# Optimization experiments

Hardware: AMD Instinct MI355X
Metric: run time of the kernel (lower is better)

The kernel has to match this reference:

```python
import jax, jax.numpy as jnp
import numpy as np

N_NODES = 100000
N_EDGES = 1000000
N_GRAPHS = 512
IN_N, IN_E, HID, OUT = 32, 16, 64, 64
EPS = 0.1  # GINEConv eps buffer (not trainable)


def _mlp2(x, w0, b0, w1, b1):
    # 2-layer MLP: Linear -> ReLU -> Linear
    return jax.nn.relu(x @ w0 + b0) @ w1 + b1


def setup_inputs() -> dict:
    key = jax.random.key(0)
    ks = jax.random.split(key, 24)
    s = 0.05
    inp = {
        "x": jax.random.normal(ks[0], (N_NODES, IN_N), jnp.float32),
        "edge_index": jax.random.randint(ks[1], (2, N_EDGES), 0, N_NODES, jnp.int32),
        "edge_attr": jax.random.normal(ks[2], (N_EDGES, IN_E), jnp.float32),
        "batch": jnp.sort(jax.random.randint(ks[3], (N_NODES,), 0, N_GRAPHS, jnp.int32)),
        # node init MLP
        "wn0": jax.random.normal(ks[4], (IN_N, HID)) * s, "bn0": jnp.zeros((HID,)),
        "wn1": jax.random.normal(ks[5], (HID, HID)) * s, "bn1": jnp.zeros((HID,)),
        # edge init MLP
        "we0": jax.random.normal(ks[6], (IN_E, HID)) * s, "be0": jnp.zeros((HID,)),
        "we1": jax.random.normal(ks[7], (HID, HID)) * s, "be1": jnp.zeros((HID,)),
        # 3 residual GINE convs, MLP weights stacked on leading layer axis
        "cw0": jax.random.normal(ks[8], (3, HID, HID)) * s, "cb0": jnp.zeros((3, HID)),
        "cw1": jax.random.normal(ks[9], (3, HID, HID)) * s, "cb1": jnp.zeros((3, HID)),
        # final GINE conv MLP (hidden -> out)
        "lw0": jax.random.normal(ks[10], (HID, HID)) * s, "lb0": jnp.zeros((HID,)),
        "lw1": jax.random.normal(ks[11], (HID, OUT)) * s, "lb1": jnp.zeros((OUT,)),
    }
    return inp


def _gine_conv(x, src, dst, e, w0, b0, w1, b1):
    # message = relu(x_j + edge_attr); aggregate = scatter-add at target i
    msg = jax.nn.relu(x[src] + e)                       # [E, H]
    agg = jax.ops.segment_sum(msg, dst, num_segments=x.shape[0])  # [N, H]
    out = agg + (1.0 + EPS) * x
    return _mlp2(out, w0, b0, w1, b1)


def reference(x, edge_index, edge_attr, batch,
              wn0, bn0, wn1, bn1, we0, be0, we1, be1,
              cw0, cb0, cw1, cb1, lw0, lb0, lw1, lb1):
    src, dst = edge_index[0], edge_index[1]
    h = _mlp2(x, wn0, bn0, wn1, bn1)          # [N, HID]
    e = _mlp2(edge_attr, we0, be0, we1, be1)  # [E, HID]
    for l in range(3):  # residual GINE layers (BatchNorm never applied in source forward)
        h = jax.nn.relu(h + _gine_conv(h, src, dst, e, cw0[l], cb0[l], cw1[l], cb1[l]))
    h = _gine_conv(h, src, dst, e, lw0, lb0, lw1, lb1)  # [N, OUT]
    return jax.ops.segment_sum(h, batch, num_segments=N_GRAPHS)  # global_add_pool -> [G, OUT]
```

## Files before the change

### kernel.cpp

```cpp
#include <hip/hip_runtime.h>
#include <hip/hip_bf16.h>
#include <stdint.h>

#define N_NODES 100000
#define N_EDGES 1000000
#define N_GRAPHS 512
#define HID 64
#define INN 32
#define INE 16
#define CPAD 32

#define NPB 256
#define NBKT ((N_NODES + NPB - 1) / NPB)
#define BCAP 4096

typedef unsigned int uint32;
typedef unsigned short ushort16;
typedef __attribute__((ext_vector_type(8))) short bf8;
typedef __attribute__((ext_vector_type(4))) float f32x4;

__device__ __forceinline__ ushort16 f2bf(float f) {
    uint32 u = __float_as_uint(f);
    uint32 r = (u + 0x7fffu + ((u >> 16) & 1u)) >> 16;
    return (ushort16)r;
}
__device__ __forceinline__ uint32 pack_bf2(float lo, float hi) {
    return (uint32)f2bf(lo) | ((uint32)f2bf(hi) << 16);
}
__device__ __forceinline__ float bf_lo(uint32 v) { return __uint_as_float(v << 16); }
__device__ __forceinline__ float bf_hi(uint32 v) { return __uint_as_float(v & 0xffff0000u); }


__global__ void k_diag(float* out, float val) { out[threadIdx.x] = val; }


__global__ __launch_bounds__(256) void k_binA(const int* __restrict__ src,
                                              const int* __restrict__ dst,
                                              int* __restrict__ bcursor,
                                              uint2* __restrict__ binned) {
    __shared__ int cnt[NBKT];
    __shared__ int cur[NBKT];
    const int t = threadIdx.x;
    for (int b = t; b < NBKT; b += 256) cnt[b] = 0;
    __syncthreads();
    const int base = blockIdx.x * 4096;
    #pragma unroll
    for (int j = 0; j < 16; j++) {
        int e = base + j * 256 + t;
        if (e < N_EDGES) atomicAdd(&cnt[dst[e] >> 8], 1);
    }
    __syncthreads();
    for (int b = t; b < NBKT; b += 256) {
        int c = cnt[b];
        cur[b] = (c > 0) ? atomicAdd(&bcursor[(size_t)b * CPAD], c) : 0;
    }
    __syncthreads();
    #pragma unroll
    for (int j = 0; j < 16; j++) {
        int e = base + j * 256 + t;
        if (e < N_EDGES) {
            int d = dst[e];
            int bkt = d >> 8;
            int r = atomicAdd(&cur[bkt], 1);
            if (r < BCAP)
                binned[(size_t)bkt * BCAP + r] =
                    make_uint2((uint32)src[e] | ((uint32)(d & (NPB - 1)) << 17), (uint32)e);
        }
    }
}

__global__ __launch_bounds__(512) void k_scanB(const int* __restrict__ bcursor,
                                               int* __restrict__ bbase) {
    __shared__ int sh[512];
    const int t = threadIdx.x;
    int v = (t < NBKT) ? min(bcursor[(size_t)t * CPAD], BCAP) : 0;
    sh[t] = v; __syncthreads();
    for (int off = 1; off < 512; off <<= 1) {
        int u = (t >= off) ? sh[t - off] : 0;
        __syncthreads();
        sh[t] += u;
        __syncthreads();
    }
    if (t < NBKT) bbase[t] = sh[t] - v;
}

__global__ __launch_bounds__(256) void k_bucketB(const int* __restrict__ bcursor,
                                                 const int* __restrict__ bbase,
                                                 const uint2* __restrict__ binned,
                                                 int* __restrict__ rowptr,
                                                 int* __restrict__ perm_src,
                                                 int* __restrict__ eperm) {
    __shared__ int cnt[NPB];
    __shared__ int sh[NPB];
    const int b = blockIdx.x, t = threadIdx.x;
    const int n = min(bcursor[(size_t)b * CPAD], BCAP);
    const int base = bbase[b];
    const uint2* brec = binned + (size_t)b * BCAP;
    cnt[t] = 0;
    __syncthreads();
    for (int i = t; i < n; i += 256)
        atomicAdd(&cnt[brec[i].x >> 17], 1);
    __syncthreads();
    int c = cnt[t];
    sh[t] = c; __syncthreads();
    for (int off = 1; off < NPB; off <<= 1) {
        int u = (t >= off) ? sh[t - off] : 0;
        __syncthreads();
        sh[t] += u;
        __syncthreads();
    }
    int excl = sh[t] - c;
    int g = b * NPB + t;
    if (g < N_NODES) rowptr[g] = base + excl;
    if (b == 0 && t == 0) rowptr[N_NODES] = N_EDGES;
    cnt[t] = excl;
    __syncthreads();
    for (int i = t; i < n; i += 256) {
        uint2 r = brec[i];
        int dl = (int)(r.x >> 17);
        int p = base + atomicAdd(&cnt[dl], 1);
        perm_src[p] = (int)(r.x & 0x1FFFFu);
        eperm[p] = (int)r.y;
    }
}


template<int K0, bool RELU_RES, bool BF_IN>
__global__ __launch_bounds__(256, 3) void k_mlp_mfma(
    const void* __restrict__ in, const float* __restrict__ hprev, float* __restrict__ out,
    const float* __restrict__ w0, const float* __restrict__ b0,
    const float* __restrict__ w1, const float* __restrict__ b1,
    uint32* __restrict__ out_bf, int nrows)
{
    constexpr int NF = K0 / 32;
    __shared__ ushort tile[4][16 * 72];
    const int wave = threadIdx.x >> 6, lane = threadIdx.x & 63;
    const int quad = lane >> 4, mn = lane & 15;
    ushort* T = &tile[wave][0];

    bf8 w0f[4][NF];
    #pragma unroll
    for (int t = 0; t < 4; t++)
        #pragma unroll
        for (int f = 0; f < NF; f++)
            #pragma unroll
            for (int j = 0; j < 8; j++) {
                int k = f * 32 + quad * 8 + j;
                w0f[t][f][j] = (short)f2bf(w0[k * HID + t * 16 + mn]);
            }
    bf8 w1f[4][2];
    #pragma unroll
    for (int t = 0; t < 4; t++)
        #pragma unroll
        for (int f = 0; f < 2; f++)
            #pragma unroll
            for (int j = 0; j < 8; j++) {
                int k = f * 32 + quad * 8 + j;
                w1f[t][f][j] = (short)f2bf(w1[k * HID + t * 16 + mn]);
            }
    float b0v[4], b1v[4];
    #pragma unroll
    for (int t = 0; t < 4; t++) { b0v[t] = b0[t*16+mn]; b1v[t] = b1[t*16+mn]; }

    const int ebase = blockIdx.x * 64 + wave * 16;
    int rowA = ebase + mn; if (rowA > nrows - 1) rowA = nrows - 1;
    bf8 a1[NF];
    if (BF_IN) {
        const ushort* row = (const ushort*)in + (size_t)rowA * HID;
        #pragma unroll
        for (int f = 0; f < NF; f++)
            a1[f] = *(const bf8*)(row + f * 32 + quad * 8);
    } else {
        const float* inf = (const float*)in;
        #pragma unroll
        for (int f = 0; f < NF; f++) {
            const float4* pr = (const float4*)(inf + (size_t)rowA * K0 + f * 32 + quad * 8);
            float4 v0 = pr[0], v1 = pr[1];
            a1[f][0]=(short)f2bf(v0.x); a1[f][1]=(short)f2bf(v0.y);
            a1[f][2]=(short)f2bf(v0.z); a1[f][3]=(short)f2bf(v0.w);
            a1[f][4]=(short)f2bf(v1.x); a1[f][5]=(short)f2bf(v1.y);
            a1[f][6]=(short)f2bf(v1.z); a1[f][7]=(short)f2bf(v1.w);
        }
    }
    #pragma unroll
    for (int t = 0; t < 4; t++) {
        f32x4 c = {0.f, 0.f, 0.f, 0.f};
        #pragma unroll
        for (int f = 0; f < NF; f++)
            c = __builtin_amdgcn_mfma_f32_16x16x32_bf16(a1[f], w0f[t][f], c, 0, 0, 0);
        #pragma unroll
        for (int rg = 0; rg < 4; rg++) {
            int row = quad * 4 + rg;
            T[row * 72 + t * 16 + mn] = f2bf(fmaxf(c[rg] + b0v[t], 0.f));
        }
    }
    __syncthreads();
    bf8 a2[2];
    #pragma unroll
    for (int f = 0; f < 2; f++)
        a2[f] = *(const bf8*)&T[mn * 72 + f * 32 + quad * 8];
    #pragma unroll
    for (int t = 0; t < 4; t++) {
        f32x4 c = {0.f, 0.f, 0.f, 0.f};
        c = __builtin_amdgcn_mfma_f32_16x16x32_bf16(a2[0], w1f[t][0], c, 0, 0, 0);
        c = __builtin_amdgcn_mfma_f32_16x16x32_bf16(a2[1], w1f[t][1], c, 0, 0, 0);
        #pragma unroll
        for (int rg = 0; rg < 4; rg++) {
            int row = quad * 4 + rg;
            int rowg = ebase + row;
            int rowc = (rowg < nrows) ? rowg : (nrows - 1);
            float v = c[rg] + b1v[t];
            if (RELU_RES) {
                float hv = hprev[(size_t)rowc * HID + t * 16 + mn];
                v = fmaxf(v + hv, 0.f);
            }
            if (rowg < nrows) out[(size_t)rowg * HID + t * 16 + mn] = v;
            T[row * 72 + t * 16 + mn] = f2bf(v);
        }
    }
    if (out_bf) {
        __syncthreads();
        int half = lane >> 5, c32 = lane & 31;
        #pragma unroll
        for (int rr = 0; rr < 8; rr++) {
            int row = rr * 2 + half;
            int pos = ebase + row;
            if (pos < nrows) {
                uint32 lo = T[row * 72 + c32 * 2];
                uint32 hi = T[row * 72 + c32 * 2 + 1];
                out_bf[(size_t)pos * 32 + c32] = lo | (hi << 16);
            }
        }
    }
}


__global__ __launch_bounds__(256, 4) void k_edge_mlp_mfma(
    const float* __restrict__ eattr, const int* __restrict__ eperm,
    uint32* __restrict__ e_sorted,
    const float* __restrict__ w0, const float* __restrict__ b0,
    const float* __restrict__ w1, const float* __restrict__ b1)
{
    __shared__ ushort tile[4][16 * 72];
    const int wave = threadIdx.x >> 6, lane = threadIdx.x & 63;
    const int quad = lane >> 4, mn = lane & 15;
    ushort* T = &tile[wave][0];

    bf8 w0f[4];
    #pragma unroll
    for (int t = 0; t < 4; t++) {
        #pragma unroll
        for (int j = 0; j < 8; j++) {
            int k = quad * 8 + j;
            float v = (k < INE) ? w0[k * HID + t * 16 + mn] : 0.f;
            w0f[t][j] = (short)f2bf(v);
        }
    }
    bf8 w1f[4][2];
    #pragma unroll
    for (int t = 0; t < 4; t++)
        #pragma unroll
        for (int f = 0; f < 2; f++)
            #pragma unroll
            for (int j = 0; j < 8; j++) {
                int k = f * 32 + quad * 8 + j;
                w1f[t][f][j] = (short)f2bf(w1[k * HID + t * 16 + mn]);
            }
    float b0v[4], b1v[4];
    #pragma unroll
    for (int t = 0; t < 4; t++) { b0v[t] = b0[t*16+mn]; b1v[t] = b1[t*16+mn]; }

    const int nChunks = N_EDGES / 64;
    for (int chunk = blockIdx.x; chunk < nChunks; chunk += gridDim.x) {
        const int ebase = chunk * 64 + wave * 16;
        const int erow = eperm[ebase + mn];
        bf8 a1 = {};
        if (quad < 2) {
            const float4* pr = (const float4*)(eattr + (size_t)erow * INE + quad * 8);
            float4 v0 = pr[0], v1 = pr[1];
            a1[0]=(short)f2bf(v0.x); a1[1]=(short)f2bf(v0.y);
            a1[2]=(short)f2bf(v0.z); a1[3]=(short)f2bf(v0.w);
            a1[4]=(short)f2bf(v1.x); a1[5]=(short)f2bf(v1.y);
            a1[6]=(short)f2bf(v1.z); a1[7]=(short)f2bf(v1.w);
        }
        #pragma unroll
        for (int t = 0; t < 4; t++) {
            f32x4 c = {0.f, 0.f, 0.f, 0.f};
            c = __builtin_amdgcn_mfma_f32_16x16x32_bf16(a1, w0f[t], c, 0, 0, 0);
            #pragma unroll
            for (int rg = 0; rg < 4; rg++) {
                int row = quad * 4 + rg;
                T[row * 72 + t * 16 + mn] = f2bf(fmaxf(c[rg] + b0v[t], 0.f));
            }
        }
        __syncthreads();
        bf8 a2[2];
        #pragma unroll
        for (int f = 0; f < 2; f++)
            a2[f] = *(const bf8*)&T[mn * 72 + f * 32 + quad * 8];
        #pragma unroll
        for (int t = 0; t < 4; t++) {
            f32x4 c = {0.f, 0.f, 0.f, 0.f};
            c = __builtin_amdgcn_mfma_f32_16x16x32_bf16(a2[0], w1f[t][0], c, 0, 0, 0);
            c = __builtin_amdgcn_mfma_f32_16x16x32_bf16(a2[1], w1f[t][1], c, 0, 0, 0);
            #pragma unroll
            for (int rg = 0; rg < 4; rg++) {
                int row = quad * 4 + rg;
                T[row * 72 + t * 16 + mn] = f2bf(c[rg] + b1v[t]);
            }
        }
        __syncthreads();
        int half = lane >> 5, c32 = lane & 31;
        #pragma unroll
        for (int rr = 0; rr < 8; rr++) {
            int row = rr * 2 + half;
            int drow = ebase + row;
            uint32 lo = T[row * 72 + c32 * 2];
            uint32 hi = T[row * 72 + c32 * 2 + 1];
            e_sorted[(size_t)drow * 32 + c32] = lo | (hi << 16);
        }
        __syncthreads();
    }
}


__global__ __launch_bounds__(256, 4) void k_agg(
    const float* __restrict__ h, const uint32* __restrict__ h_bf,
    const uint32* __restrict__ e_sorted,
    const int* __restrict__ rowptr, const int* __restrict__ perm_src,
    uint32* __restrict__ z_bf)
{
    int node = blockIdx.x * 4 + (threadIdx.x >> 6);
    if (node >= N_NODES) return;
    int lane = threadIdx.x & 63;
    int half = lane >> 5, c = lane & 31;
    int r0 = rowptr[node], r1 = rowptr[node + 1];
    const float2 hn = *(const float2*)&h[(size_t)node * HID + 2*c];
    float accx = 0.f, accy = 0.f;
    #pragma unroll 1
    for (int base = r0; base < r1; base += 16) {
        int idxs[8]; int sidx[8];
        #pragma unroll
        for (int j = 0; j < 8; j++) {
            int idx = base + 2*j + half;
            idxs[j] = idx;
            int idxc = (idx < r1) ? idx : (r1 - 1);
            sidx[j] = perm_src[idxc];
        }
        uint32 hv[8], ev[8];
        #pragma unroll
        for (int j = 0; j < 8; j++) {
            int idxc = (idxs[j] < r1) ? idxs[j] : (r1 - 1);
            hv[j] = h_bf[(size_t)sidx[j] * 32 + c];
            ev[j] = e_sorted[(size_t)idxc * 32 + c];
        }
        #pragma unroll
        for (int j = 0; j < 8; j++) {
            float mx = fmaxf(bf_lo(hv[j]) + bf_lo(ev[j]), 0.f);
            float my = fmaxf(bf_hi(hv[j]) + bf_hi(ev[j]), 0.f);
            if (idxs[j] < r1) { accx += mx; accy += my; }
        }
    }
    accx += __shfl_xor(accx, 32);
    accy += __shfl_xor(accy, 32);
    if (half == 0) {
        float rx = fmaf(1.1f, hn.x, accx);
        float ry = fmaf(1.1f, hn.y, accy);
        z_bf[(size_t)node * 32 + c] = pack_bf2(rx, ry);
    }
}


__global__ __launch_bounds__(256) void k_pool(
    const float* __restrict__ h, const int* __restrict__ batch, float* __restrict__ out)
{
    int g = blockIdx.x;
    int lane = threadIdx.x & 63, wave = threadIdx.x >> 6;
    int lo = 0, hi = N_NODES;
    while (lo < hi) { int mid = (lo + hi) >> 1; if (batch[mid] < g) lo = mid + 1; else hi = mid; }
    int start = lo;
    hi = N_NODES;
    while (lo < hi) { int mid = (lo + hi) >> 1; if (batch[mid] < g + 1) lo = mid + 1; else hi = mid; }
    int end = lo;
    float acc = 0.f;
    for (int n = start + wave; n < end; n += 4)
        acc += h[(size_t)n*HID + lane];
    __shared__ float sh[4][64];
    sh[wave][lane] = acc;
    __syncthreads();
    if (wave == 0)
        out[(size_t)g*HID + lane] = sh[0][lane] + sh[1][lane] + sh[2][lane] + sh[3][lane];
}


extern "C" void kernel_launch(void* const* d_in, const int* in_sizes, int n_in,
                              void* d_out, int out_size, void* d_ws, size_t ws_size,
                              hipStream_t stream) {
    const float* x     = (const float*)d_in[0];
    const int*   eidx  = (const int*)  d_in[1];
    const float* eattr = (const float*)d_in[2];
    const int*   batch = (const int*)  d_in[3];
    const float* wn0 = (const float*)d_in[4];  const float* bn0 = (const float*)d_in[5];
    const float* wn1 = (const float*)d_in[6];  const float* bn1 = (const float*)d_in[7];
    const float* we0 = (const float*)d_in[8];  const float* be0 = (const float*)d_in[9];
    const float* we1 = (const float*)d_in[10]; const float* be1 = (const float*)d_in[11];
    const float* cw0 = (const float*)d_in[12]; const float* cb0 = (const float*)d_in[13];
    const float* cw1 = (const float*)d_in[14]; const float* cb1 = (const float*)d_in[15];
    const float* lw0 = (const float*)d_in[16]; const float* lb0 = (const float*)d_in[17];
    const float* lw1 = (const float*)d_in[18]; const float* lb1 = (const float*)d_in[19];
    const int* src = eidx;
    const int* dst = eidx + N_EDGES;

    char* ws = (char*)d_ws;
    size_t off = 0;
    auto alloc = [&](size_t bytes) -> void* {
        void* p = ws + off;
        off = (off + bytes + 255) & ~(size_t)255;
        return p;
    };
    int*    bcursor  = (int*)  alloc((size_t)NBKT * CPAD * 4);
    int*    bbase    = (int*)  alloc((size_t)NBKT * 4);
    uint2*  binned   = (uint2*)alloc((size_t)NBKT * BCAP * 8);
    int*    rowptr   = (int*)  alloc((size_t)(N_NODES + 1) * 4);
    int*    perm_src = (int*)  alloc((size_t)N_EDGES * 4);
    int*    eperm    = (int*)  alloc((size_t)N_EDGES * 4);
    float*  h        = (float*)alloc((size_t)N_NODES * HID * 4);
    uint32* z_bf     = (uint32*)alloc((size_t)N_NODES * 32 * 4);
    uint32* h_bf     = (uint32*)alloc((size_t)N_NODES * 32 * 4);
    uint32* e_sorted = (uint32*)alloc((size_t)N_EDGES * HID * 2);
    if (off > ws_size) {
        k_diag<<<1, 64, 0, stream>>>((float*)d_out, 1.0e9f);
        return;
    }

    hipMemsetAsync(bcursor, 0, (size_t)NBKT * CPAD * 4, stream);
    k_binA<<<(N_EDGES + 4095) / 4096, 256, 0, stream>>>(src, dst, bcursor, binned);
    k_scanB<<<1, 512, 0, stream>>>(bcursor, bbase);
    k_bucketB<<<NBKT, 256, 0, stream>>>(bcursor, bbase, binned, rowptr, perm_src, eperm);

    const int MGRID = (N_NODES + 63) / 64;

    k_mlp_mfma<INN, false, false><<<MGRID, 256, 0, stream>>>(x, nullptr, h, wn0, bn0, wn1, bn1,
                                                             h_bf, N_NODES);

    k_edge_mlp_mfma<<<1024, 256, 0, stream>>>(eattr, eperm, e_sorted,
                                              we0, be0, we1, be1);

    const int AGRID = (N_NODES + 3) / 4;
    for (int l = 0; l < 3; l++) {
        k_agg<<<AGRID, 256, 0, stream>>>(h, h_bf, e_sorted, rowptr, perm_src, z_bf);
        k_mlp_mfma<HID, true, true><<<MGRID, 256, 0, stream>>>(z_bf, h, h,
                                                               cw0 + l * 4096, cb0 + l * 64,
                                                               cw1 + l * 4096, cb1 + l * 64,
                                                               h_bf, N_NODES);
    }
    k_agg<<<AGRID, 256, 0, stream>>>(h, h_bf, e_sorted, rowptr, perm_src, z_bf);
    k_mlp_mfma<HID, false, true><<<MGRID, 256, 0, stream>>>(z_bf, nullptr, h,
                                                            lw0, lb0, lw1, lb1, nullptr, N_NODES);

    k_pool<<<N_GRAPHS, 256, 0, stream>>>(h, batch, (float*)d_out);
}
```

Baseline: 518.5 us.

## Prepack MLP weights into bf16 MFMA fragments and pipeline edge MLP loads

Adds a one-block prep kernel that converts all MLP weight matrices once per call into bf16 MFMA fragment layout, so each MLP block loads ready-made fragments instead of doing strided fp32 gathers and conversions. Block-wide __syncthreads are replaced with wave barriers, since each wave only uses its own LDS tile. The edge MLP is reworked to process 16-row tiles per wave with software-prefetched eperm indices and edge attributes one iteration ahead, and its grid is doubled. LDS reads are widened to 32-bit. The cost is one extra small kernel launch and slightly more register pressure from prefetching.

After: 512.6 us. No clear change (-1.1%).

```diff
diff --git a/kernel.cpp b/kernel.cpp
--- a/kernel.cpp
+++ b/kernel.cpp
@@ -14,6 +14,16 @@
 #define NBKT ((N_NODES + NPB - 1) / NPB)
 #define BCAP 4096
 
+#define S_NW0 0
+#define S_NW1 4
+#define S_EW0 12
+#define S_EW1 16
+#define S_CW0 24
+#define S_CW1 48
+#define S_LW0 72
+#define S_LW1 80
+#define NSLOT 88
+
 typedef unsigned int uint32;
 typedef unsigned short ushort16;
 typedef __attribute__((ext_vector_type(8))) short bf8;
@@ -32,6 +42,39 @@
 
 
 __global__ void k_diag(float* out, float val) { out[threadIdx.x] = val; }
+
+
+__global__ __launch_bounds__(256) void k_prep(
+    const float* __restrict__ wn0, const float* __restrict__ wn1,
+    const float* __restrict__ we0, const float* __restrict__ we1,
+    const float* __restrict__ cw0, const float* __restrict__ cw1,
+    const float* __restrict__ lw0, const float* __restrict__ lw1,
+    uint32* __restrict__ wfrag)
+{
+    for (int idx = threadIdx.x; idx < NSLOT * 64; idx += 256) {
+        int s = idx >> 6, lane = idx & 63;
+        const float* w; int K, NF, base;
+        if (s < 4)       { w = wn0; K = 32; NF = 1; base = S_NW0; }
+        else if (s < 12) { w = wn1; K = 64; NF = 2; base = S_NW1; }
+        else if (s < 16) { w = we0; K = 16; NF = 1; base = S_EW0; }
+        else if (s < 24) { w = we1; K = 64; NF = 2; base = S_EW1; }
+        else if (s < 48) { int l = (s - S_CW0) >> 3; w = cw0 + l * 4096; K = 64; NF = 2; base = S_CW0 + l * 8; }
+        else if (s < 72) { int l = (s - S_CW1) >> 3; w = cw1 + l * 4096; K = 64; NF = 2; base = S_CW1 + l * 8; }
+        else if (s < 80) { w = lw0; K = 64; NF = 2; base = S_LW0; }
+        else             { w = lw1; K = 64; NF = 2; base = S_LW1; }
+        int r = s - base, t = r / NF, f = r - t * NF;
+        int quad = lane >> 4, mn = lane & 15;
+        uint32 out[4];
+        #pragma unroll
+        for (int p = 0; p < 4; p++) {
+            int k0 = f * 32 + quad * 8 + p * 2;
+            float lo = (k0 < K)     ? w[(size_t)k0 * HID + t * 16 + mn]       : 0.f;
+            float hi = (k0 + 1 < K) ? w[(size_t)(k0 + 1) * HID + t * 16 + mn] : 0.f;
+            out[p] = pack_bf2(lo, hi);
+        }
+        *(uint4*)(wfrag + (size_t)idx * 4) = make_uint4(out[0], out[1], out[2], out[3]);
+    }
+}
 
 
 __global__ __launch_bounds__(256) void k_binA(const int* __restrict__ src,
@@ -125,14 +168,13 @@
 }
 
 
-template<int K0, bool RELU_RES, bool BF_IN>
+template<int NF, bool RELU_RES, bool BF_IN>
 __global__ __launch_bounds__(256, 3) void k_mlp_mfma(
     const void* __restrict__ in, const float* __restrict__ hprev, float* __restrict__ out,
-    const float* __restrict__ w0, const float* __restrict__ b0,
-    const float* __restrict__ w1, const float* __restrict__ b1,
+    const uint32* __restrict__ wf0, const float* __restrict__ b0,
+    const uint32* __restrict__ wf1, const float* __restrict__ b1,
     uint32* __restrict__ out_bf, int nrows)
 {
-    constexpr int NF = K0 / 32;
     __shared__ ushort tile[4][16 * 72];
     const int wave = threadIdx.x >> 6, lane = threadIdx.x & 63;
     const int quad = lane >> 4, mn = lane & 15;
@@ -143,21 +185,13 @@
     for (int t = 0; t < 4; t++)
         #pragma unroll
         for (int f = 0; f < NF; f++)
-            #pragma unroll
-            for (int j = 0; j < 8; j++) {
-                int k = f * 32 + quad * 8 + j;
-                w0f[t][f][j] = (short)f2bf(w0[k * HID + t * 16 + mn]);
-            }
+            w0f[t][f] = *(const bf8*)(wf0 + ((size_t)(t * NF + f) * 64 + lane) * 4);
     bf8 w1f[4][2];
     #pragma unroll
     for (int t = 0; t < 4; t++)
         #pragma unroll
         for (int f = 0; f < 2; f++)
-            #pragma unroll
-            for (int j = 0; j < 8; j++) {
-                int k = f * 32 + quad * 8 + j;
-                w1f[t][f][j] = (short)f2bf(w1[k * HID + t * 16 + mn]);
-            }
+            w1f[t][f] = *(const bf8*)(wf1 + ((size_t)(t * 2 + f) * 64 + lane) * 4);
     float b0v[4], b1v[4];
     #pragma unroll
     for (int t = 0; t < 4; t++) { b0v[t] = b0[t*16+mn]; b1v[t] = b1[t*16+mn]; }
@@ -174,7 +208,7 @@
         const float* inf = (const float*)in;
         #pragma unroll
         for (int f = 0; f < NF; f++) {
-            const float4* pr = (const float4*)(inf + (size_t)rowA * K0 + f * 32 + quad * 8);
+            const float4* pr = (const float4*)(inf + (size_t)rowA * (NF * 32) + f * 32 + quad * 8);
             float4 v0 = pr[0], v1 = pr[1];
             a1[f][0]=(short)f2bf(v0.x); a1[f][1]=(short)f2bf(v0.y);
             a1[f][2]=(short)f2bf(v0.z); a1[f][3]=(short)f2bf(v0.w);
@@ -194,7 +228,7 @@
             T[row * 72 + t * 16 + mn] = f2bf(fmaxf(c[rg] + b0v[t], 0.f));
         }
     }
-    __syncthreads();
+    __builtin_amdgcn_wave_barrier();
     bf8 a2[2];
     #pragma unroll
     for (int f = 0; f < 2; f++)
@@ -219,16 +253,15 @@
         }
     }
     if (out_bf) {
-        __syncthreads();
+        __builtin_amdgcn_wave_barrier();
         int half = lane >> 5, c32 = lane & 31;
         #pragma unroll
         for (int rr = 0; rr < 8; rr++) {
             int row = rr * 2 + half;
             int pos = ebase + row;
             if (pos < nrows) {
-                uint32 lo = T[row * 72 + c32 * 2];
-                uint32 hi = T[row * 72 + c32 * 2 + 1];
-                out_bf[(size_t)pos * 32 + c32] = lo | (hi << 16);
+                uint32 w = *(const uint32*)&T[row * 72 + c32 * 2];
+                out_bf[(size_t)pos * 32 + c32] = w;
             }
         }
     }
@@ -237,9 +270,8 @@
 
 __global__ __launch_bounds__(256, 4) void k_edge_mlp_mfma(
     const float* __restrict__ eattr, const int* __restrict__ eperm,
-    uint32* __restrict__ e_sorted,
-    const float* __restrict__ w0, const float* __restrict__ b0,
-    const float* __restrict__ w1, const float* __restrict__ b1)
+    uint32* __restrict__ e_sorted, const uint32* __restrict__ wfrag,
+    const float* __restrict__ b0, const float* __restrict__ b1)
 {
     __shared__ ushort tile[4][16 * 72];
     const int wave = threadIdx.x >> 6, lane = threadIdx.x & 63;
@@ -248,78 +280,82 @@
 
     bf8 w0f[4];
     #pragma unroll
-    for (int t = 0; t < 4; t++) {
-        #pragma unroll
-        for (int j = 0; j < 8; j++) {
-            int k = quad * 8 + j;
-            float v = (k < INE) ? w0[k * HID + t * 16 + mn] : 0.f;
-            w0f[t][j] = (short)f2bf(v);
-        }
-    }
+    for (int t = 0; t < 4; t++)
+        w0f[t] = *(const bf8*)(wfrag + ((size_t)(S_EW0 + t) * 64 + lane) * 4);
     bf8 w1f[4][2];
     #pragma unroll
     for (int t = 0; t < 4; t++)
         #pragma unroll
         for (int f = 0; f < 2; f++)
-            #pragma unroll
-            for (int j = 0; j < 8; j++) {
-                int k = f * 32 + quad * 8 + j;
-                w1f[t][f][j] = (short)f2bf(w1[k * HID + t * 16 + mn]);
-            }
+            w1f[t][f] = *(const bf8*)(wfrag + ((size_t)(S_EW1 + t * 2 + f) * 64 + lane) * 4);
     float b0v[4], b1v[4];
     #pragma unroll
     for (int t = 0; t < 4; t++) { b0v[t] = b0[t*16+mn]; b1v[t] = b1[t*16+mn]; }
 
-    const int nChunks = N_EDGES / 64;
-    for (int chunk = blockIdx.x; chunk < nChunks; chunk += gridDim.x) {
-        const int ebase = chunk * 64 + wave * 16;
-        const int erow = eperm[ebase + mn];
+    const int nT = N_EDGES / 16;
+    const int stride = gridDim.x * 4;
+    int t = blockIdx.x * 4 + wave;
+
+    int ep0 = (t < nT) ? eperm[t * 16 + mn] : 0;
+    int ep1 = (t + stride < nT) ? eperm[(t + stride) * 16 + mn] : 0;
+    float4 va = make_float4(0.f,0.f,0.f,0.f), vb = va;
+    if (quad < 2 && t < nT) {
+        const float4* pr = (const float4*)(eattr + (size_t)ep0 * INE + quad * 8);
+        va = pr[0]; vb = pr[1];
+    }
+
+    for (; t < nT; t += stride) {
+        const int tn = t + stride;
+        float4 na = make_float4(0.f,0.f,0.f,0.f), nb = na;
+        if (quad < 2 && tn < nT) {
+            const float4* pr = (const float4*)(eattr + (size_t)ep1 * INE + quad * 8);
+            na = pr[0]; nb = pr[1];
+        }
+        int ep2 = (t + 2 * stride < nT) ? eperm[(t + 2 * stride) * 16 + mn] : 0;
+
         bf8 a1 = {};
         if (quad < 2) {
-            const float4* pr = (const float4*)(eattr + (size_t)erow * INE + quad * 8);
-            float4 v0 = pr[0], v1 = pr[1];
-            a1[0]=(short)f2bf(v0.x); a1[1]=(short)f2bf(v0.y);
-            a1[2]=(short)f2bf(v0.z); a1[3]=(short)f2bf(v0.w);
-            a1[4]=(short)f2bf(v1.x); a1[5]=(short)f2bf(v1.y);
-            a1[6]=(short)f2bf(v1.z); a1[7]=(short)f2bf(v1.w);
-        }
-        #pragma unroll
-        for (int t = 0; t < 4; t++) {
+            a1[0]=(short)f2bf(va.x); a1[1]=(short)f2bf(va.y);
+            a1[2]=(short)f2bf(va.z); a1[3]=(short)f2bf(va.w);
+            a1[4]=(short)f2bf(vb.x); a1[5]=(short)f2bf(vb.y);
+            a1[6]=(short)f2bf(vb.z); a1[7]=(short)f2bf(vb.w);
+        }
+        #pragma unroll
+        for (int t4 = 0; t4 < 4; t4++) {
             f32x4 c = {0.f, 0.f, 0.f, 0.f};
-            c = __builtin_amdgcn_mfma_f32_16x16x32_bf16(a1, w0f[t], c, 0, 0, 0);
+            c = __builtin_amdgcn_mfma_f32_16x16x32_bf16(a1, w0f[t4], c, 0, 0, 0);
             #pragma unroll
             for (int rg = 0; rg < 4; rg++) {
                 int row = quad * 4 + rg;
-                T[row * 72 + t * 16 + mn] = f2bf(fmaxf(c[rg] + b0v[t], 0.f));
+                T[row * 72 + t4 * 16 + mn] = f2bf(fmaxf(c[rg] + b0v[t4], 0.f));
             }
         }
-        __syncthreads();
+        __builtin_amdgcn_wave_barrier();
         bf8 a2[2];
         #pragma unroll
         for (int f = 0; f < 2; f++)
             a2[f] = *(const bf8*)&T[mn * 72 + f * 32 + quad * 8];
         #pragma unroll
-        for (int t = 0; t < 4; t++) {
+        for (int t4 = 0; t4 < 4; t4++) {
             f32x4 c = {0.f, 0.f, 0.f, 0.f};
-            c = __builtin_amdgcn_mfma_f32_16x16x32_bf16(a2[0], w1f[t][0], c, 0, 0, 0);
-            c = __builtin_amdgcn_mfma_f32_16x16x32_bf16(a2[1], w1f[t][1], c, 0, 0, 0);
+            c = __builtin_amdgcn_mfma_f32_16x16x32_bf16(a2[0], w1f[t4][0], c, 0, 0, 0);
+            c = __builtin_amdgcn_mfma_f32_16x16x32_bf16(a2[1], w1f[t4][1], c, 0, 0, 0);
             #pragma unroll
             for (int rg = 0; rg < 4; rg++) {
                 int row = quad * 4 + rg;
-                T[row * 72 + t * 16 + mn] = f2bf(c[rg] + b1v[t]);
+                T[row * 72 + t4 * 16 + mn] = f2bf(c[rg] + b1v[t4]);
             }
         }
-        __syncthreads();
+        __builtin_amdgcn_wave_barrier();
         int half = lane >> 5, c32 = lane & 31;
         #pragma unroll
         for (int rr = 0; rr < 8; rr++) {
             int row = rr * 2 + half;
-            int drow = ebase + row;
-            uint32 lo = T[row * 72 + c32 * 2];
-            uint32 hi = T[row * 72 + c32 * 2 + 1];
-            e_sorted[(size_t)drow * 32 + c32] = lo | (hi << 16);
-        }
-        __syncthreads();
+            uint32 w = *(const uint32*)&T[row * 72 + c32 * 2];
+            e_sorted[((size_t)t * 16 + row) * 32 + c32] = w;
+        }
+        __builtin_amdgcn_wave_barrier();
+        va = na; vb = nb; ep1 = ep2;
     }
 }
 
@@ -428,10 +464,13 @@
     uint32* z_bf     = (uint32*)alloc((size_t)N_NODES * 32 * 4);
     uint32* h_bf     = (uint32*)alloc((size_t)N_NODES * 32 * 4);
     uint32* e_sorted = (uint32*)alloc((size_t)N_EDGES * HID * 2);
+    uint32* wfrag    = (uint32*)alloc((size_t)NSLOT * 64 * 16);
     if (off > ws_size) {
         k_diag<<<1, 64, 0, stream>>>((float*)d_out, 1.0e9f);
         return;
     }
+
+    k_prep<<<1, 256, 0, stream>>>(wn0, wn1, we0, we1, cw0, cw1, lw0, lw1, wfrag);
 
     hipMemsetAsync(bcursor, 0, (size_t)NBKT * CPAD * 4, stream);
     k_binA<<<(N_EDGES + 4095) / 4096, 256, 0, stream>>>(src, dst, bcursor, binned);
@@ -440,23 +479,21 @@
 
     const int MGRID = (N_NODES + 63) / 64;
 
-    k_mlp_mfma<INN, false, false><<<MGRID, 256, 0, stream>>>(x, nullptr, h, wn0, bn0, wn1, bn1,
-                                                             h_bf, N_NODES);
-
-    k_edge_mlp_mfma<<<1024, 256, 0, stream>>>(eattr, eperm, e_sorted,
-                                              we0, be0, we1, be1);
+    k_mlp_mfma<1, false, false><<<MGRID, 256, 0, stream>>>(
+        x, nullptr, h, wfrag + S_NW0 * 256, bn0, wfrag + S_NW1 * 256, bn1, h_bf, N_NODES);
+
+    k_edge_mlp_mfma<<<2048, 256, 0, stream>>>(eattr, eperm, e_sorted, wfrag, be0, be1);
 
     const int AGRID = (N_NODES + 3) / 4;
     for (int l = 0; l < 3; l++) {
         k_agg<<<AGRID, 256, 0, stream>>>(h, h_bf, e_sorted, rowptr, perm_src, z_bf);
-        k_mlp_mfma<HID, true, true><<<MGRID, 256, 0, stream>>>(z_bf, h, h,
-                                                               cw0 + l * 4096, cb0 + l * 64,
-                                                               cw1 + l * 4096, cb1 + l * 64,
-                                                               h_bf, N_NODES);
+        k_mlp_mfma<2, true, true><<<MGRID, 256, 0, stream>>>(
+            z_bf, h, h, wfrag + (S_CW0 + l * 8) * 256, cb0 + l * 64,
+            wfrag + (S_CW1 + l * 8) * 256, cb1 + l * 64, h_bf, N_NODES);
     }
     k_agg<<<AGRID, 256, 0, stream>>>(h, h_bf, e_sorted, rowptr, perm_src, z_bf);
-    k_mlp_mfma<HID, false, true><<<MGRID, 256, 0, stream>>>(z_bf, nullptr, h,
-                                                            lw0, lb0, lw1, lb1, nullptr, N_NODES);
+    k_mlp_mfma<2, false, true><<<MGRID, 256, 0, stream>>>(
+        z_bf, nullptr, h, wfrag + S_LW0 * 256, lb0, wfrag + S_LW1 * 256, lb1, nullptr, N_NODES);
 
     k_pool<<<N_GRAPHS, 256, 0, stream>>>(h, batch, (float*)d_out);
 }
```
